# Kernel optimization log

Hardware: AMD Instinct MI355X
Metric: run time of the kernel (lower is better)

The kernel has to match this reference:

```python
import jax, jax.numpy as jnp
import numpy as np

VOCAB, D, H1, H2, T = 32000, 256, 256, 256, 12
PAD, START, STOP = 0, 10, 11
B, S, NS = 32, 512, 16


def setup_inputs() -> dict:
    key = jax.random.key(0)
    ks = jax.random.split(key, 16)
    def rn(k, shape, scale=0.1):
        return (jax.random.normal(k, shape) * scale).astype(jnp.float32)
    inputs = jax.random.randint(ks[0], (B, S), 0, VOCAB)
    sent_embs = jax.random.normal(ks[1], (B, NS, 2 * H1), dtype=jnp.float32)
    embed = rn(ks[2], (VOCAB, D)).at[0].set(0.0)  # padding_idx=0
    # BiLSTM 1: input D, hidden H1; gate order i,f,g,o; dim 0 = [fwd, bwd]
    lstm1_wih = rn(ks[3], (2, 4 * H1, D))
    lstm1_whh = rn(ks[4], (2, 4 * H1, H1))
    lstm1_b = rn(ks[5], (2, 4 * H1))  # b_ih + b_hh fused
    # BiLSTM 2: input 4*H1 (= 2*2*lstm1_units), hidden H2
    lstm2_wih = rn(ks[6], (2, 4 * H2, 4 * H1))
    lstm2_whh = rn(ks[7], (2, 4 * H2, H2))
    lstm2_b = rn(ks[8], (2, 4 * H2))
    attW = rn(ks[9], (2 * H1, 2 * H1))
    h2t_w = rn(ks[10], (T, 2 * H2))
    h2t_b = rn(ks[11], (T,))
    trans = jax.random.normal(ks[12], (T, T), dtype=jnp.float32)
    trans = trans.at[START, :].set(-10000.0).at[:, STOP].set(-10000.0)
    return dict(inputs=inputs, sent_embs=sent_embs, embed=embed,
                lstm1_wih=lstm1_wih, lstm1_whh=lstm1_whh, lstm1_b=lstm1_b,
                lstm2_wih=lstm2_wih, lstm2_whh=lstm2_whh, lstm2_b=lstm2_b,
                attW=attW, h2t_w=h2t_w, h2t_b=h2t_b, trans=trans)


def _lstm_dir(x, wih, whh, b, reverse=False):
    # x: (S, B, Din) -> (S, B, H)
    if reverse:
        x = x[::-1]
    Hh = whh.shape[1]
    Bn = x.shape[1]
    def step(carry, xt):
        h, c = carry
        gates = xt @ wih.T + h @ whh.T + b
        i, f, g, o = jnp.split(gates, 4, axis=-1)
        c = jax.nn.sigmoid(f) * c + jax.nn.sigmoid(i) * jnp.tanh(g)
        h = jax.nn.sigmoid(o) * jnp.tanh(c)
        return (h, c), h
    init = (jnp.zeros((Bn, Hh), x.dtype), jnp.zeros((Bn, Hh), x.dtype))
    _, hs = jax.lax.scan(step, init, x)
    return hs[::-1] if reverse else hs


def _bilstm(x, wih, whh, b):
    fwd = _lstm_dir(x, wih[0], whh[0], b[0])
    bwd = _lstm_dir(x, wih[1], whh[1], b[1], reverse=True)
    return jnp.concatenate([fwd, bwd], axis=-1)


def _lstm_features(inputs, sent_embs, embed, lstm1_wih, lstm1_whh, lstm1_b,
                   lstm2_wih, lstm2_whh, lstm2_b, attW, h2t_w, h2t_b):
    emb = embed[inputs].transpose(1, 0, 2)            # (S,B,D); dropout is identity at eval
    l1 = _bilstm(emb, lstm1_wih, lstm1_whh, lstm1_b)  # (S,B,2H1)
    word = l1.transpose(1, 0, 2)                      # (B,S,2H1)
    wx = jnp.einsum('bse,fe->bsf', word, attW)        # Linear W (no bias)
    scores = jnp.einsum('bsf,bnf->bsn', wx, sent_embs)
    aw = jax.nn.softmax(scores, axis=-1)
    g = jnp.einsum('bsn,bnf->bsf', aw, sent_embs)
    comb = jnp.concatenate([wx, g], axis=-1)          # (B,S,4H1)
    l2 = _bilstm(comb.transpose(1, 0, 2), lstm2_wih, lstm2_whh, lstm2_b)  # (S,B,2H2)
    feats = jnp.einsum('sbf,tf->bst', l2, h2t_w) + h2t_b  # (B,S,T)
    return feats


def _viterbi(feats_b, trans):
    # feats_b: (S,T) -> (path (S,), score)
    init = jnp.full((T,), -10000.0, feats_b.dtype).at[START].set(0.0)
    def step(fv, feat):
        sc = fv[None, :] + trans          # [next, prev]
        bp = jnp.argmax(sc, axis=1)
        return jnp.max(sc, axis=1) + feat, bp
    fv, bps = jax.lax.scan(step, init, feats_b)
    term = fv + trans[STOP]
    best = jnp.argmax(term)
    def back(tag, bp):
        return bp[tag], tag
    _, path = jax.lax.scan(back, best, bps, reverse=True)
    return path, term[best]


def reference(inputs, sent_embs, embed, lstm1_wih, lstm1_whh, lstm1_b,
              lstm2_wih, lstm2_whh, lstm2_b, attW, h2t_w, h2t_b, trans):
    feats = _lstm_features(inputs, sent_embs, embed, lstm1_wih, lstm1_whh, lstm1_b,
                           lstm2_wih, lstm2_whh, lstm2_b, attW, h2t_w, h2t_b)
    paths, _ = jax.vmap(_viterbi, in_axes=(0, None))(feats, trans)
    return paths  # (B,S) predicted tag sequence
```

## Files before the change

### kernel.cpp

```cpp
#include <hip/hip_runtime.h>
#include <hip/hip_bf16.h>

#define BB 32
#define SS 512
#define DD 256
#define HH 256
#define GG 1024
#define MM (SS*BB)
#define NSENT 16
#define TT 12
#define TAG_START 10
#define TAG_STOP 11

typedef unsigned long long u64;
typedef unsigned int u32;

__device__ __forceinline__ float sigm(float x) {
  x = fminf(fmaxf(x, -15.f), 15.f);
  return 1.f / (1.f + __expf(-x));
}
__device__ __forceinline__ float tanh_fast(float x) {
  x = fminf(fmaxf(x, -15.f), 15.f);
  float e = __expf(2.f * x);
  return (e - 1.f) / (e + 1.f);
}

__global__ void embed_kernel(const int* __restrict__ toks, const float* __restrict__ emb,
                             float* __restrict__ X1) {
  int m = blockIdx.x;
  int s = m >> 5, b = m & 31;
  int tok = toks[b * SS + s];
  ((float4*)(X1 + (size_t)m * DD))[threadIdx.x] =
      ((const float4*)(emb + (size_t)tok * DD))[threadIdx.x];
}

__launch_bounds__(256)
__global__ void gemm_nt(const float* __restrict__ A, const float* __restrict__ W_,
                        const float* __restrict__ bias_, float* __restrict__ C_,
                        int K, int lda, int ldw, int ldC, size_t wz, size_t cz) {
  __shared__ float As[16 * 132];
  __shared__ float Ws[16 * 132];
  const float* W = W_ + (size_t)blockIdx.z * wz;
  const float* bias = bias_ ? bias_ + (size_t)blockIdx.z * GG : nullptr;
  float* C = C_ + (size_t)blockIdx.z * cz;
  const int tid = threadIdx.x;
  const int n0 = blockIdx.x * 128, m0 = blockIdx.y * 128;
  const int row = tid & 127, half = tid >> 7;
  const int tx = tid & 15, ty = tid >> 4;
  float acc[8][8] = {};
  const float* Arow = A + (size_t)(m0 + row) * lda;
  const float* Wrow = W + (size_t)(n0 + row) * ldw;
  for (int kk = 0; kk < K; kk += 16) {
    const int kb = half * 8;
    float4 a0 = *(const float4*)(Arow + kk + kb);
    float4 a1 = *(const float4*)(Arow + kk + kb + 4);
    float4 w0 = *(const float4*)(Wrow + kk + kb);
    float4 w1 = *(const float4*)(Wrow + kk + kb + 4);
    As[(kb + 0) * 132 + row] = a0.x; As[(kb + 1) * 132 + row] = a0.y;
    As[(kb + 2) * 132 + row] = a0.z; As[(kb + 3) * 132 + row] = a0.w;
    As[(kb + 4) * 132 + row] = a1.x; As[(kb + 5) * 132 + row] = a1.y;
    As[(kb + 6) * 132 + row] = a1.z; As[(kb + 7) * 132 + row] = a1.w;
    Ws[(kb + 0) * 132 + row] = w0.x; Ws[(kb + 1) * 132 + row] = w0.y;
    Ws[(kb + 2) * 132 + row] = w0.z; Ws[(kb + 3) * 132 + row] = w0.w;
    Ws[(kb + 4) * 132 + row] = w1.x; Ws[(kb + 5) * 132 + row] = w1.y;
    Ws[(kb + 6) * 132 + row] = w1.z; Ws[(kb + 7) * 132 + row] = w1.w;
    __syncthreads();
#pragma unroll
    for (int kl = 0; kl < 16; ++kl) {
      const float4 alo = *(const float4*)&As[kl * 132 + ty * 4];
      const float4 ahi = *(const float4*)&As[kl * 132 + 64 + ty * 4];
      const float4 wlo = *(const float4*)&Ws[kl * 132 + tx * 4];
      const float4 whi = *(const float4*)&Ws[kl * 132 + 64 + tx * 4];
      const float am[8] = {alo.x, alo.y, alo.z, alo.w, ahi.x, ahi.y, ahi.z, ahi.w};
      const float wm[8] = {wlo.x, wlo.y, wlo.z, wlo.w, whi.x, whi.y, whi.z, whi.w};
#pragma unroll
      for (int i = 0; i < 8; ++i)
#pragma unroll
        for (int j = 0; j < 8; ++j) acc[i][j] = fmaf(am[i], wm[j], acc[i][j]);
    }
    __syncthreads();
  }
  float4 blo = make_float4(0.f, 0.f, 0.f, 0.f), bhi = blo;
  if (bias) {
    blo = *(const float4*)(bias + n0 + tx * 4);
    bhi = *(const float4*)(bias + n0 + 64 + tx * 4);
  }
#pragma unroll
  for (int i = 0; i < 8; ++i) {
    const int m = m0 + ((i < 4) ? (ty * 4 + i) : (64 + ty * 4 + i - 4));
    float4 lo = make_float4(acc[i][0] + blo.x, acc[i][1] + blo.y,
                            acc[i][2] + blo.z, acc[i][3] + blo.w);
    float4 hi = make_float4(acc[i][4] + bhi.x, acc[i][5] + bhi.y,
                            acc[i][6] + bhi.z, acc[i][7] + bhi.w);
    *(float4*)(C + (size_t)m * ldC + n0 + tx * 4) = lo;
    *(float4*)(C + (size_t)m * ldC + n0 + 64 + tx * 4) = hi;
  }
}

__global__ void prep_whh(const float* __restrict__ whh1, const float* __restrict__ whh2,
                         float* __restrict__ o1, float* __restrict__ o2) {
  int idx0 = blockIdx.x * 256 + threadIdx.x;
  int layer = idx0 >> 19;
  int idx = idx0 & 524287;
  const float* whh = layer ? whh2 : whh1;
  float* out = layer ? o2 : o1;
  int pos = idx & 255;
  int r = (idx >> 8) & 127;
  int sl = (idx >> 15) & 7;
  int dir = idx >> 18;
  int ki = pos & 3;
  int k4 = (pos >> 2) ^ (r & 63);
  int k = k4 * 4 + ki;
  int g = (r >> 5) * 256 + sl * 32 + (r & 31);
  out[idx] = whh[(size_t)(dir * GG + g) * HH + k];
}

__launch_bounds__(128)
__global__ void rec_kernel(const float* __restrict__ Xp, const float* __restrict__ whh_p,
                           float* __restrict__ hist, u64* __restrict__ hx,
                           const float* __restrict__ aw, const float* __restrict__ sentW,
                           int useAtt) {
  __shared__ float whh_lds[32768];
  __shared__ float h_lds[512];
  __shared__ float g_lds[256];
  const int tid = threadIdx.x;
  const int bid = blockIdx.x;
  const int sl = bid >> 5;
  const int db = bid & 31;
  const int d = db & 1;
  const int bg = db >> 1;
  const int r = tid;
  const int swz = r & 63;
  const float* wp = whh_p + (size_t)(d * 8 + sl) * 32768;
  for (int i = tid * 4; i < 32768; i += 512)
    *(float4*)&whh_lds[i] = *(const float4*)&wp[i];
  const float* XpD = Xp + (size_t)d * MM * GG;
  const int gcol = (r >> 5) * 256 + sl * 32 + (r & 31);
  const int jj = tid & 31, cc = tid >> 5;
  const int hc = tid >> 6, hk = (tid & 63) * 4;
  const int histMine = (((tid & 63) >> 3) == sl);
  float creg = 0.f;
  float sw0[16], sw1[16];
  if (useAtt) {
    const float* swp = sentW + ((size_t)d * 512 + (size_t)(bg * 2) * 16) * 1024 + gcol;
#pragma unroll
    for (int n = 0; n < 16; ++n) {
      sw0[n] = swp[(size_t)n * 1024];
      sw1[n] = swp[(size_t)(16 + n) * 1024];
    }
  }
  u64* grp[2] = { hx + ((size_t)(0 * 2 + d) * 16 + bg) * 512,
                  hx + ((size_t)(1 * 2 + d) * 16 + bg) * 512 };
  __syncthreads();
  for (int t = 0; t < SS; ++t) {
    const int s = d ? (SS - 1 - t) : t;
    const int m0 = s * BB + bg * 2;
    float xp0 = XpD[(size_t)m0 * GG + gcol];
    float xp1 = XpD[(size_t)(m0 + 1) * GG + gcol];
    if (useAtt) {
      const float* a0 = aw + (size_t)m0 * 16;
#pragma unroll
      for (int n = 0; n < 16; ++n) {
        xp0 = fmaf(a0[n], sw0[n], xp0);
        xp1 = fmaf(a0[16 + n], sw1[n], xp1);
      }
    }
    u64 w0, w1, w2, w3;
    {
      u64* base = grp[t & 1] + tid * 4;
      w0 = __hip_atomic_load(base + 0, __ATOMIC_RELAXED, __HIP_MEMORY_SCOPE_AGENT);
      w1 = __hip_atomic_load(base + 1, __ATOMIC_RELAXED, __HIP_MEMORY_SCOPE_AGENT);
      w2 = __hip_atomic_load(base + 2, __ATOMIC_RELAXED, __HIP_MEMORY_SCOPE_AGENT);
      w3 = __hip_atomic_load(base + 3, __ATOMIC_RELAXED, __HIP_MEMORY_SCOPE_AGENT);
      while (((u32)(w0 >> 32) != (u32)t) | ((u32)(w1 >> 32) != (u32)t) |
             ((u32)(w2 >> 32) != (u32)t) | ((u32)(w3 >> 32) != (u32)t)) {
        __builtin_amdgcn_s_sleep(1);
        w0 = __hip_atomic_load(base + 0, __ATOMIC_RELAXED, __HIP_MEMORY_SCOPE_AGENT);
        w1 = __hip_atomic_load(base + 1, __ATOMIC_RELAXED, __HIP_MEMORY_SCOPE_AGENT);
        w2 = __hip_atomic_load(base + 2, __ATOMIC_RELAXED, __HIP_MEMORY_SCOPE_AGENT);
        w3 = __hip_atomic_load(base + 3, __ATOMIC_RELAXED, __HIP_MEMORY_SCOPE_AGENT);
      }
    }
    *(float4*)&h_lds[tid * 4] = make_float4(
        __uint_as_float((u32)w0), __uint_as_float((u32)w1),
        __uint_as_float((u32)w2), __uint_as_float((u32)w3));
    if (histMine && t > 0) {
      const int sp = d ? (SS - t) : (t - 1);
      *(float4*)&hist[(size_t)(sp * BB + bg * 2 + hc) * 512 + d * 256 + hk] =
          make_float4(__uint_as_float((u32)w0), __uint_as_float((u32)w1),
                      __uint_as_float((u32)w2), __uint_as_float((u32)w3));
    }
    __syncthreads();
    {
      float acc0 = 0.f, acc1 = 0.f;
#pragma unroll 8
      for (int k4 = 0; k4 < 64; ++k4) {
        const float4 w = *(const float4*)&whh_lds[r * 256 + ((k4 ^ swz) << 2)];
        const float4 h0 = *(const float4*)&h_lds[k4 * 4];
        const float4 h1 = *(const float4*)&h_lds[256 + k4 * 4];
        acc0 = fmaf(w.x, h0.x, acc0); acc0 = fmaf(w.y, h0.y, acc0);
        acc0 = fmaf(w.z, h0.z, acc0); acc0 = fmaf(w.w, h0.w, acc0);
        acc1 = fmaf(w.x, h1.x, acc1); acc1 = fmaf(w.y, h1.y, acc1);
        acc1 = fmaf(w.z, h1.z, acc1); acc1 = fmaf(w.w, h1.w, acc1);
      }
      *(float2*)&g_lds[r * 2] = make_float2(acc0 + xp0, acc1 + xp1);
    }
    __syncthreads();
    if (tid < 64) {
      const float iv = g_lds[(jj) * 2 + cc];
      const float fv = g_lds[(32 + jj) * 2 + cc];
      const float gv = g_lds[(64 + jj) * 2 + cc];
      const float ov = g_lds[(96 + jj) * 2 + cc];
      const float cs = sigm(fv) * creg + sigm(iv) * tanh_fast(gv);
      creg = cs;
      const float hn = sigm(ov) * tanh_fast(cs);
      u64 w = ((u64)(u32)(t + 1) << 32) | (u64)__float_as_uint(hn);
      __hip_atomic_store(grp[(t + 1) & 1] + cc * 256 + sl * 32 + jj, w,
                         __ATOMIC_RELAXED, __HIP_MEMORY_SCOPE_AGENT);
    }
  }
  if (histMine) {
    u64* base = grp[SS & 1] + tid * 4;
    u64 w0, w1, w2, w3;
    do {
      w0 = __hip_atomic_load(base + 0, __ATOMIC_RELAXED, __HIP_MEMORY_SCOPE_AGENT);
      w1 = __hip_atomic_load(base + 1, __ATOMIC_RELAXED, __HIP_MEMORY_SCOPE_AGENT);
      w2 = __hip_atomic_load(base + 2, __ATOMIC_RELAXED, __HIP_MEMORY_SCOPE_AGENT);
      w3 = __hip_atomic_load(base + 3, __ATOMIC_RELAXED, __HIP_MEMORY_SCOPE_AGENT);
      if (((u32)(w0 >> 32) == (u32)SS) & ((u32)(w1 >> 32) == (u32)SS) &
          ((u32)(w2 >> 32) == (u32)SS) & ((u32)(w3 >> 32) == (u32)SS)) break;
      __builtin_amdgcn_s_sleep(1);
    } while (true);
    const int sp = d ? 0 : (SS - 1);
    *(float4*)&hist[(size_t)(sp * BB + bg * 2 + hc) * 512 + d * 256 + hk] =
        make_float4(__uint_as_float((u32)w0), __uint_as_float((u32)w1),
                    __uint_as_float((u32)w2), __uint_as_float((u32)w3));
  }
}

__global__ void aw_kernel(const float* __restrict__ wx, const float* __restrict__ sent,
                          float* __restrict__ awout) {
  __shared__ float sl[NSENT * 512];
  __shared__ float wxr[512];
  __shared__ float parts[256];
  __shared__ float avals[NSENT];
  __shared__ float red0;
  const int tid = threadIdx.x;
  const int b = blockIdx.y;
  const int s0 = blockIdx.x * 32;
  for (int i = tid; i < NSENT * 512; i += 256) sl[i] = sent[(size_t)b * NSENT * 512 + i];
  __syncthreads();
  for (int si = 0; si < 32; ++si) {
    const int m = (s0 + si) * BB + b;
    for (int i = tid; i < 512; i += 256) wxr[i] = wx[(size_t)m * 512 + i];
    __syncthreads();
    const int n = tid >> 4, kp = tid & 15;
    float p = 0.f;
#pragma unroll 8
    for (int f = kp * 32; f < kp * 32 + 32; ++f) p = fmaf(wxr[f], sl[n * 512 + f], p);
    parts[tid] = p;
    __syncthreads();
    if (tid < NSENT) {
      float sc = 0.f;
      for (int qq = 0; qq < 16; ++qq) sc += parts[tid * 16 + qq];
      avals[tid] = sc;
    }
    __syncthreads();
    if (tid == 0) {
      float mx = avals[0];
      for (int qq = 1; qq < NSENT; ++qq) mx = fmaxf(mx, avals[qq]);
      float sm = 0.f;
      for (int qq = 0; qq < NSENT; ++qq) { float e = expf(avals[qq] - mx); avals[qq] = e; sm += e; }
      red0 = 1.f / sm;
    }
    __syncthreads();
    if (tid < NSENT) awout[(size_t)m * 16 + tid] = avals[tid] * red0;
    __syncthreads();
  }
}

__global__ void feats_kernel(const float* __restrict__ l2m, const float* __restrict__ w,
                             const float* __restrict__ bias, float* __restrict__ feats) {
  const int wave = threadIdx.x >> 6, lane = threadIdx.x & 63;
  const int m = blockIdx.x * 4 + wave;
  const float* row = l2m + (size_t)m * 512;
  float rv[8];
#pragma unroll
  for (int i = 0; i < 8; ++i) rv[i] = row[lane + i * 64];
  for (int t = 0; t < TT; ++t) {
    const float* wr = w + t * 512;
    float p = 0.f;
#pragma unroll
    for (int i = 0; i < 8; ++i) p = fmaf(rv[i], wr[lane + i * 64], p);
#pragma unroll
    for (int off = 32; off; off >>= 1) p += __shfl_down(p, off);
    if (lane == 0) feats[(size_t)m * TT + t] = p + bias[t];
  }
}

__global__ void viterbi_kernel(const float* __restrict__ feats, const float* __restrict__ trans,
                               int* __restrict__ out) {
  __shared__ float flds[SS * TT];
  __shared__ unsigned char bp[SS * TT];
  __shared__ float tr[TT * TT];
  __shared__ float fv[TT];
  __shared__ float tv[TT];
  __shared__ int pathS[SS];
  const int b = blockIdx.x, tid = threadIdx.x;
  for (int i = tid; i < SS * TT; i += 64) {
    int s = i / TT, t = i - s * TT;
    flds[i] = feats[(size_t)(s * BB + b) * TT + t];
  }
  for (int i = tid; i < TT * TT; i += 64) tr[i] = trans[i];
  if (tid < TT) fv[tid] = (tid == TAG_START) ? 0.f : -10000.f;
  __syncthreads();
  for (int s = 0; s < SS; ++s) {
    float nf = 0.f;
    if (tid < TT) {
      float mx = -1e30f;
      int bj = 0;
#pragma unroll
      for (int jj = 0; jj < TT; ++jj) {
        float v = fv[jj] + tr[tid * TT + jj];
        if (v > mx) { mx = v; bj = jj; }
      }
      nf = mx + flds[s * TT + tid];
      bp[s * TT + tid] = (unsigned char)bj;
    }
    __syncthreads();
    if (tid < TT) fv[tid] = nf;
    __syncthreads();
  }
  if (tid < TT) tv[tid] = fv[tid] + tr[TAG_STOP * TT + tid];
  __syncthreads();
  if (tid == 0) {
    int best = 0;
    float mx = tv[0];
    for (int jj = 1; jj < TT; ++jj)
      if (tv[jj] > mx) { mx = tv[jj]; best = jj; }
    pathS[SS - 1] = best;
    for (int s = SS - 1; s > 0; --s) { best = bp[s * TT + best]; pathS[s - 1] = best; }
  }
  __syncthreads();
  for (int s = tid; s < SS; s += 64) out[b * SS + s] = pathS[s];
}

#define OFF_XP    ((size_t)0)
#define OFF_WX    ((size_t)134217728)
#define OFF_L2M   ((size_t)167772160)
#define OFF_WORD  ((size_t)201326592)
#define OFF_WT1   ((size_t)234881024)
#define OFF_WT2   ((size_t)236978176)
#define OFF_FEATS ((size_t)239075328)
#define OFF_HX1   ((size_t)239861760)
#define OFF_HX2   ((size_t)240123904)
#define OFF_SENTW ((size_t)240386048)
#define OFF_AW    ((size_t)244580352)

extern "C" void kernel_launch(void* const* d_in, const int* in_sizes, int n_in,
                              void* d_out, int out_size, void* d_ws, size_t ws_size,
                              hipStream_t stream) {
  const int* inputs  = (const int*)d_in[0];
  const float* sent  = (const float*)d_in[1];
  const float* emb   = (const float*)d_in[2];
  const float* l1wih = (const float*)d_in[3];
  const float* l1whh = (const float*)d_in[4];
  const float* l1b   = (const float*)d_in[5];
  const float* l2wih = (const float*)d_in[6];
  const float* l2whh = (const float*)d_in[7];
  const float* l2b   = (const float*)d_in[8];
  const float* attW  = (const float*)d_in[9];
  const float* h2tw  = (const float*)d_in[10];
  const float* h2tb  = (const float*)d_in[11];
  const float* trans = (const float*)d_in[12];
  int* out = (int*)d_out;
  char* ws = (char*)d_ws;

  float* Xp    = (float*)(ws + OFF_XP);
  float* wx    = (float*)(ws + OFF_WX);
  float* l2m   = (float*)(ws + OFF_L2M);
  float* X1    = l2m;
  float* word  = (float*)(ws + OFF_WORD);
  float* wt1   = (float*)(ws + OFF_WT1);
  float* wt2   = (float*)(ws + OFF_WT2);
  float* feats = (float*)(ws + OFF_FEATS);
  u64* hx1     = (u64*)(ws + OFF_HX1);
  u64* hx2     = (u64*)(ws + OFF_HX2);
  float* sentW = (float*)(ws + OFF_SENTW);
  float* awb   = (float*)(ws + OFF_AW);

  hipMemsetAsync(ws + OFF_HX1, 0, 262144 * 2, stream);

  prep_whh<<<4096, 256, 0, stream>>>(l1whh, l2whh, wt1, wt2);
  gemm_nt<<<dim3(8, 4, 2), 256, 0, stream>>>(sent, l2wih + 512, nullptr, sentW,
                                             512, 512, GG, 1024,
                                             (size_t)GG * GG, (size_t)512 * 1024);
  embed_kernel<<<MM, 64, 0, stream>>>(inputs, emb, X1);
  gemm_nt<<<dim3(8, 128, 2), 256, 0, stream>>>(X1, l1wih, l1b, Xp,
                                               DD, DD, DD, GG,
                                               (size_t)GG * DD, (size_t)MM * GG);
  rec_kernel<<<256, 128, 0, stream>>>(Xp, wt1, word, hx1, nullptr, nullptr, 0);
  gemm_nt<<<dim3(4, 128, 1), 256, 0, stream>>>(word, attW, nullptr, wx,
                                               512, 512, 512, 512, 0, 0);
  aw_kernel<<<dim3(16, 32), 256, 0, stream>>>(wx, sent, awb);
  gemm_nt<<<dim3(8, 128, 2), 256, 0, stream>>>(wx, l2wih, l2b, Xp,
                                               512, 512, GG, GG,
                                               (size_t)GG * GG, (size_t)MM * GG);
  rec_kernel<<<256, 128, 0, stream>>>(Xp, wt2, l2m, hx2, awb, sentW, 1);
  feats_kernel<<<MM / 4, 256, 0, stream>>>(l2m, h2tw, h2tb, feats);
  viterbi_kernel<<<BB, 64, 0, stream>>>(feats, trans, out);
}
```

Baseline: 4.623 ms.

## Keep recurrent weight slices in registers instead of LDS

Each thread of the recurrent kernel now holds its 256 weights of the recurrent matrix in registers for all 512 steps, instead of re-reading them from LDS every step. The prep kernel writes the weights in a new interleaved layout so the one-time load into registers is coalesced. The inner dot product is fully unrolled with four split accumulators for more instruction-level parallelism, and launch bounds allow one block per CU so the kernel can use a very large register budget. The goal is to remove per-step LDS bandwidth on the serial recurrence path, at the risk of register spills or higher register pressure around the spin-wait code.

Result: slower. 9.778 ms (+111.5%).

```diff
diff --git a/kernel.cpp b/kernel.cpp
--- a/kernel.cpp
+++ b/kernel.cpp
@@ -104,23 +104,21 @@
   int idx = idx0 & 524287;
   const float* whh = layer ? whh2 : whh1;
   float* out = layer ? o2 : o1;
-  int pos = idx & 255;
-  int r = (idx >> 8) & 127;
+  int c  = idx & 3;
+  int r  = (idx >> 2) & 127;
+  int i4 = (idx >> 9) & 63;
   int sl = (idx >> 15) & 7;
-  int dir = idx >> 18;
-  int ki = pos & 3;
-  int k4 = (pos >> 2) ^ (r & 63);
-  int k = k4 * 4 + ki;
-  int g = (r >> 5) * 256 + sl * 32 + (r & 31);
-  out[idx] = whh[(size_t)(dir * GG + g) * HH + k];
-}
-
-__launch_bounds__(128)
+  int d  = idx >> 18;
+  int g  = (r >> 5) * 256 + sl * 32 + (r & 31);
+  int k  = i4 * 4 + c;
+  out[idx] = whh[(size_t)(d * GG + g) * HH + k];
+}
+
+__launch_bounds__(128, 1)
 __global__ void rec_kernel(const float* __restrict__ Xp, const float* __restrict__ whh_p,
                            float* __restrict__ hist, u64* __restrict__ hx,
                            const float* __restrict__ aw, const float* __restrict__ sentW,
                            int useAtt) {
-  __shared__ float whh_lds[32768];
   __shared__ float h_lds[512];
   __shared__ float g_lds[256];
   const int tid = threadIdx.x;
@@ -130,10 +128,14 @@
   const int d = db & 1;
   const int bg = db >> 1;
   const int r = tid;
-  const int swz = r & 63;
   const float* wp = whh_p + (size_t)(d * 8 + sl) * 32768;
-  for (int i = tid * 4; i < 32768; i += 512)
-    *(float4*)&whh_lds[i] = *(const float4*)&wp[i];
+  float w[256];
+#pragma unroll
+  for (int i4 = 0; i4 < 64; ++i4) {
+    const float4 v = *(const float4*)&wp[(i4 * 128 + r) * 4];
+    w[i4 * 4 + 0] = v.x; w[i4 * 4 + 1] = v.y;
+    w[i4 * 4 + 2] = v.z; w[i4 * 4 + 3] = v.w;
+  }
   const float* XpD = Xp + (size_t)d * MM * GG;
   const int gcol = (r >> 5) * 256 + sl * 32 + (r & 31);
   const int jj = tid & 31, cc = tid >> 5;
@@ -151,7 +153,7 @@
   }
   u64* grp[2] = { hx + ((size_t)(0 * 2 + d) * 16 + bg) * 512,
                   hx + ((size_t)(1 * 2 + d) * 16 + bg) * 512 };
-  __syncthreads();
+#pragma unroll 1
   for (int t = 0; t < SS; ++t) {
     const int s = d ? (SS - 1 - t) : t;
     const int m0 = s * BB + bg * 2;
@@ -192,18 +194,23 @@
     }
     __syncthreads();
     {
-      float acc0 = 0.f, acc1 = 0.f;
-#pragma unroll 8
-      for (int k4 = 0; k4 < 64; ++k4) {
-        const float4 w = *(const float4*)&whh_lds[r * 256 + ((k4 ^ swz) << 2)];
-        const float4 h0 = *(const float4*)&h_lds[k4 * 4];
-        const float4 h1 = *(const float4*)&h_lds[256 + k4 * 4];
-        acc0 = fmaf(w.x, h0.x, acc0); acc0 = fmaf(w.y, h0.y, acc0);
-        acc0 = fmaf(w.z, h0.z, acc0); acc0 = fmaf(w.w, h0.w, acc0);
-        acc1 = fmaf(w.x, h1.x, acc1); acc1 = fmaf(w.y, h1.y, acc1);
-        acc1 = fmaf(w.z, h1.z, acc1); acc1 = fmaf(w.w, h1.w, acc1);
+      float a00 = 0.f, a01 = 0.f, a10 = 0.f, a11 = 0.f;
+#pragma unroll
+      for (int k8 = 0; k8 < 32; ++k8) {
+        const float4 h0a = *(const float4*)&h_lds[k8 * 8];
+        const float4 h0b = *(const float4*)&h_lds[k8 * 8 + 4];
+        const float4 h1a = *(const float4*)&h_lds[256 + k8 * 8];
+        const float4 h1b = *(const float4*)&h_lds[256 + k8 * 8 + 4];
+        a00 = fmaf(w[k8*8+0], h0a.x, a00); a00 = fmaf(w[k8*8+1], h0a.y, a00);
+        a00 = fmaf(w[k8*8+2], h0a.z, a00); a00 = fmaf(w[k8*8+3], h0a.w, a00);
+        a01 = fmaf(w[k8*8+4], h0b.x, a01); a01 = fmaf(w[k8*8+5], h0b.y, a01);
+        a01 = fmaf(w[k8*8+6], h0b.z, a01); a01 = fmaf(w[k8*8+7], h0b.w, a01);
+        a10 = fmaf(w[k8*8+0], h1a.x, a10); a10 = fmaf(w[k8*8+1], h1a.y, a10);
+        a10 = fmaf(w[k8*8+2], h1a.z, a10); a10 = fmaf(w[k8*8+3], h1a.w, a10);
+        a11 = fmaf(w[k8*8+4], h1b.x, a11); a11 = fmaf(w[k8*8+5], h1b.y, a11);
+        a11 = fmaf(w[k8*8+6], h1b.z, a11); a11 = fmaf(w[k8*8+7], h1b.w, a11);
       }
-      *(float2*)&g_lds[r * 2] = make_float2(acc0 + xp0, acc1 + xp1);
+      *(float2*)&g_lds[r * 2] = make_float2(a00 + a01 + xp0, a10 + a11 + xp1);
     }
     __syncthreads();
     if (tid < 64) {
@@ -214,8 +221,8 @@
       const float cs = sigm(fv) * creg + sigm(iv) * tanh_fast(gv);
       creg = cs;
       const float hn = sigm(ov) * tanh_fast(cs);
-      u64 w = ((u64)(u32)(t + 1) << 32) | (u64)__float_as_uint(hn);
-      __hip_atomic_store(grp[(t + 1) & 1] + cc * 256 + sl * 32 + jj, w,
+      u64 wv = ((u64)(u32)(t + 1) << 32) | (u64)__float_as_uint(hn);
+      __hip_atomic_store(grp[(t + 1) & 1] + cc * 256 + sl * 32 + jj, wv,
                          __ATOMIC_RELAXED, __HIP_MEMORY_SCOPE_AGENT);
     }
   }
@@ -389,7 +396,7 @@
   float* sentW = (float*)(ws + OFF_SENTW);
   float* awb   = (float*)(ws + OFF_AW);
 
-  hipMemsetAsync(ws + OFF_HX1, 0, 262144 * 2, stream);
+  (void)hipMemsetAsync(ws + OFF_HX1, 0, 262144 * 2, stream);
 
   prep_whh<<<4096, 256, 0, stream>>>(l1whh, l2whh, wt1, wt2);
   gemm_nt<<<dim3(8, 4, 2), 256, 0, stream>>>(sent, l2wih + 512, nullptr, sentW,
```
